# Performance work log

Hardware: AMD Instinct MI355X
Metric: run time of the kernel (lower is better)

Reference implementation:

```python
import jax, jax.numpy as jnp
import numpy as np
from jax import lax

HEATMAP_THRESH = 0.1


def _conv(x, w, b, stride=1):
    y = lax.conv_general_dilated(x, w, (stride, stride), 'SAME',
                                 dimension_numbers=('NCHW', 'OIHW', 'NCHW'))
    return y + b[None, :, None, None]


def _maxpool2(x):
    return lax.reduce_window(x, -jnp.inf, lax.max, (1, 1, 2, 2), (1, 1, 2, 2), 'VALID')


def _up2(x):
    return jnp.repeat(jnp.repeat(x, 2, axis=2), 2, axis=3)


def _find_peaks_mask(hm, thresh):
    # Vectorized equivalent of the CPU nested-loop _find_peaks:
    # interior pixel is a peak iff v > thresh and v >= its 4 axial neighbors.
    c = hm[:, :, 1:-1, 1:-1]
    m = ((c > thresh)
         & (c >= hm[:, :, :-2, 1:-1]) & (c >= hm[:, :, 2:, 1:-1])
         & (c >= hm[:, :, 1:-1, :-2]) & (c >= hm[:, :, 1:-1, 2:]))
    return jnp.pad(m, ((0, 0), (0, 0), (1, 1), (1, 1)))  # border never a peak


def _param(key, shape):
    fan_in = int(np.prod(shape[1:]))
    return jax.random.normal(key, shape, jnp.float32) / np.sqrt(fan_in)


_SHAPES = {
    'w_d1': (32, 3, 3, 3), 'w_d2': (64, 32, 3, 3), 'w_bn': (128, 64, 3, 3),
    'w_u1': (64, 192, 3, 3), 'w_u2': (32, 96, 3, 3), 'w_seg': (1, 32, 1, 1),
    'w_p1': (64, 4, 3, 3), 'w_p2': (128, 64, 3, 3),
    'w_hm': (17, 128, 1, 1), 'w_paf': (32, 128, 1, 1),
}


def setup_inputs() -> dict:
    key = jax.random.key(0)
    ks = jax.random.split(key, 1 + len(_SHAPES))
    B, H, W = 8, 384, 384
    inp = {'x': jax.random.normal(ks[0], (B, 3, H, W), jnp.float32)}
    for i, (n, s) in enumerate(_SHAPES.items()):
        inp[n] = _param(ks[i + 1], s)
        inp[n.replace('w_', 'b_')] = jnp.zeros((s[0],), jnp.float32)
    return inp


def _forward(x, w_d1, b_d1, w_d2, b_d2, w_bn, b_bn, w_u1, b_u1, w_u2, b_u2,
             w_seg, b_seg, w_p1, b_p1, w_p2, b_p2, w_hm, b_hm, w_paf, b_paf):
    # --- UNet segmentation ---
    d1 = jax.nn.relu(_conv(x, w_d1, b_d1))                    # [B,32,384,384]
    d2 = jax.nn.relu(_conv(_maxpool2(d1), w_d2, b_d2))        # [B,64,192,192]
    bn = jax.nn.relu(_conv(_maxpool2(d2), w_bn, b_bn))        # [B,128,96,96]
    u1 = jax.nn.relu(_conv(jnp.concatenate([_up2(bn), d2], 1), w_u1, b_u1))  # [B,64,192,192]
    u2 = jax.nn.relu(_conv(jnp.concatenate([_up2(u1), d1], 1), w_u2, b_u2))  # [B,32,384,384]
    seg = _conv(u2, w_seg, b_seg)                             # [B,1,384,384]
    # --- Pose net on image + detached seg logits ---
    xp = jnp.concatenate([x, lax.stop_gradient(seg)], axis=1)  # detach()
    p1 = jax.nn.relu(_conv(xp, w_p1, b_p1, stride=2))          # [B,64,192,192]
    p2 = jax.nn.relu(_conv(p1, w_p2, b_p2, stride=2))          # [B,128,96,96]
    hm = _conv(p2, w_hm, b_hm)                                 # [B,17,96,96]
    paf = _conv(p2, w_paf, b_paf)                              # [B,32,96,96]
    return seg, hm, paf


def reference(x, w_d1, b_d1, w_d2, b_d2, w_bn, b_bn, w_u1, b_u1, w_u2, b_u2,
              w_seg, b_seg, w_p1, b_p1, w_p2, b_p2, w_hm, b_hm, w_paf, b_paf):
    seg, hm, paf = _forward(x, w_d1, b_d1, w_d2, b_d2, w_bn, b_bn, w_u1, b_u1,
                            w_u2, b_u2, w_seg, b_seg, w_p1, b_p1, w_p2, b_p2,
                            w_hm, b_hm, w_paf, b_paf)
    # jit-friendly replacement for the variable-length python peak lists:
    # boolean mask over [B,K,h,w]; (x,y) coords recoverable via jnp.nonzero offline.
    peaks = _find_peaks_mask(hm, HEATMAP_THRESH)
    return seg, hm, paf, peaks
```

## Files before the change

kernel.cpp:

```cpp
#include <hip/hip_runtime.h>


#define BS 256
#define BSW 512

typedef _Float16 half8 __attribute__((ext_vector_type(8)));
typedef float floatx4 __attribute__((ext_vector_type(4)));

#define LDSDW 20
#define PLT8 10000
#define PLT4 6000
#define ESTR 388
#define ESTR4 196

__device__ inline void packw_gen_body(
    const float* __restrict__ w, _Float16* __restrict__ bp, int Cin, int Cout,
    int tid, int total)
{
    int lane = tid & 63;
    int t = tid >> 6;
    int NTl = Cout >> 4;
    int nt = t % NTl; t /= NTl;
    int tap = t % 9;
    int chunk = t / 9;
    int q = lane >> 4, n = lane & 15;
    int co = nt * 16 + n;
    _Float16* ph = bp + (size_t)tid * 8;
    _Float16* pl = bp + (size_t)total * 8 + (size_t)tid * 8;
#pragma unroll
    for (int j = 0; j < 8; ++j) {
        int ci = chunk * 32 + q * 8 + j;
        float v = w[((size_t)co * Cin + ci) * 9 + tap];
        _Float16 h = (_Float16)v;
        ph[j] = h;
        pl[j] = (_Float16)(v - (float)h);
    }
}

__device__ inline void packw_1x1_body(
    const float* __restrict__ w, _Float16* __restrict__ bp, int Cin, int NTl, int Cout,
    int tid, int total)
{
    int lane = tid & 63;
    int t = tid >> 6;
    int nt = t % NTl;
    int chunk = t / NTl;
    int q = lane >> 4, n = lane & 15;
    int co = nt * 16 + n;
    _Float16* ph = bp + (size_t)tid * 8;
    _Float16* pl = bp + (size_t)total * 8 + (size_t)tid * 8;
#pragma unroll
    for (int j = 0; j < 8; ++j) {
        int ci = chunk * 32 + q * 8 + j;
        float v = (co < Cout) ? w[(size_t)co * Cin + ci] : 0.f;
        _Float16 h = (_Float16)v;
        ph[j] = h;
        pl[j] = (_Float16)(v - (float)h);
    }
}

__global__ __launch_bounds__(BS) void packw_all_kernel(
    const float* __restrict__ w_u1, const float* __restrict__ w_u2,
    const float* __restrict__ w_d2, const float* __restrict__ w_bn,
    const float* __restrict__ w_p2, const float* __restrict__ w_hm,
    const float* __restrict__ w_paf,
    _Float16* __restrict__ bp_u1, _Float16* __restrict__ bp_u2,
    _Float16* __restrict__ bp_d2, _Float16* __restrict__ bp_bn,
    _Float16* __restrict__ bp_p2, _Float16* __restrict__ bp_hm,
    _Float16* __restrict__ bp_paf)
{
    int tid = blockIdx.x * BS + threadIdx.x;
    if (tid < 13824) { packw_gen_body(w_u1, bp_u1, 192, 64, tid, 13824); return; }
    tid -= 13824;
    if (tid < 3456)  { packw_gen_body(w_u2, bp_u2, 96, 32, tid, 3456); return; }
    tid -= 3456;
    if (tid < 2304)  { packw_gen_body(w_d2, bp_d2, 32, 64, tid, 2304); return; }
    tid -= 2304;
    if (tid < 9216)  { packw_gen_body(w_bn, bp_bn, 64, 128, tid, 9216); return; }
    tid -= 9216;
    if (tid < 9216)  { packw_gen_body(w_p2, bp_p2, 64, 128, tid, 9216); return; }
    tid -= 9216;
    if (tid < 512)   { packw_1x1_body(w_hm, bp_hm, 128, 2, 17, tid, 512); return; }
    tid -= 512;
    if (tid < 512)   { packw_1x1_body(w_paf, bp_paf, 128, 2, 32, tid, 512); return; }
}

template <int TCO>
__global__ __launch_bounds__(BS, 2) void conv3x3_pool_kernel(
    const float* __restrict__ inA, int Ca,
    const float* __restrict__ w, const float* __restrict__ b,
    _Float16* __restrict__ oph, _Float16* __restrict__ opl,
    int N, int H, int W, int Cout)
{
    const int W8 = W >> 3;
    const int H2 = H >> 1, W2 = W >> 1;
    int idx = blockIdx.x * BS + threadIdx.x;
    int total = N * H2 * W8;
    if (idx >= total) return;
    int x8 = idx % W8;
    int t  = idx / W8;
    int yo = t % H2;
    int n  = t / H2;
    int x0 = x8 << 3;
    const int co0 = blockIdx.y * TCO;
    const bool left_ok  = (x0 > 0);
    const bool right_ok = (x0 + 8 < W);
    const int Cin = Ca;

    float pool[TCO][4];

#pragma unroll
    for (int rr = 0; rr < 2; ++rr) {
        int y = 2 * yo + rr;
        float acc[TCO][8];
#pragma unroll
        for (int j = 0; j < TCO; ++j) {
            float bv = b[co0 + j];
#pragma unroll
            for (int p = 0; p < 8; ++p) acc[j][p] = bv;
        }

        for (int ci = 0; ci < Cin; ++ci) {
            float v[3][10];
#pragma unroll
            for (int ky = 0; ky < 3; ++ky) {
                int iy = y + ky - 1;
                if (iy < 0 || iy >= H) {
#pragma unroll
                    for (int p = 0; p < 10; ++p) v[ky][p] = 0.f;
                    continue;
                }
                const float* r = inA + ((size_t)(n * Ca + ci) * H + iy) * W;
                v[ky][0] = left_ok ? r[x0 - 1] : 0.f;
                float4 q0 = *(const float4*)(r + x0);
                float4 q1 = *(const float4*)(r + x0 + 4);
                v[ky][1] = q0.x; v[ky][2] = q0.y; v[ky][3] = q0.z; v[ky][4] = q0.w;
                v[ky][5] = q1.x; v[ky][6] = q1.y; v[ky][7] = q1.z; v[ky][8] = q1.w;
                v[ky][9] = right_ok ? r[x0 + 8] : 0.f;
            }
#pragma unroll
            for (int j = 0; j < TCO; ++j) {
                const float* wp = w + ((size_t)(co0 + j) * Cin + ci) * 9;
#pragma unroll
                for (int ky = 0; ky < 3; ++ky) {
                    float w0 = wp[ky * 3 + 0], w1 = wp[ky * 3 + 1], w2 = wp[ky * 3 + 2];
#pragma unroll
                    for (int p = 0; p < 8; ++p)
                        acc[j][p] += w0 * v[ky][p] + w1 * v[ky][p + 1] + w2 * v[ky][p + 2];
                }
            }
        }

#pragma unroll
        for (int j = 0; j < TCO; ++j) {
#pragma unroll
            for (int p4 = 0; p4 < 4; ++p4) {
                float mrow = fmaxf(fmaxf(acc[j][2 * p4], 0.f),
                                   fmaxf(acc[j][2 * p4 + 1], 0.f));
                pool[j][p4] = (rr == 0) ? mrow : fmaxf(pool[j][p4], mrow);
            }
        }
    }

#pragma unroll
    for (int p4 = 0; p4 < 4; ++p4) {
        half8 hv, lv;
#pragma unroll
        for (int j = 0; j < 8; ++j) {
            float v = pool[j][p4];
            _Float16 h = (_Float16)v;
            hv[j] = h;
            lv[j] = (_Float16)(v - (float)h);
        }
        size_t oa = ((size_t)((n * (Cout >> 3) + (co0 >> 3)) * H2 + yo) * W2
                     + (x0 >> 1) + p4) * 8;
        *(half8*)(oph + oa) = hv;
        *(half8*)(opl + oa) = lv;
    }
}

template <int CHUNKS, int NT, int HH, int WW, int OUTMODE>
__global__ __launch_bounds__(BS) void conv3x3s_mfma_kernel(
    const _Float16* __restrict__ inh, const _Float16* __restrict__ inl,
    const _Float16* __restrict__ bp,
    const float* __restrict__ bias,
    _Float16* __restrict__ osph,
    _Float16* __restrict__ ospl)
{
    constexpr int PL = 4 * 34 * LDSDW;
    constexpr int EPI = 64 * NT * 16;
    constexpr int LDS_DW = (2 * PL > EPI) ? 2 * PL : EPI;
    __shared__ unsigned int lds[LDS_DW];

    int xblks = WW / 32;
    int b = blockIdx.x;
    int xb = b % xblks; b /= xblks;
    int yp = b % (HH / 2);
    int n  = b / (HH / 2);
    int y0 = yp * 2;
    int x0 = xb * 32;

    int tid = threadIdx.x;
    int lane = tid & 63, wv = tid >> 6;
    int m = lane & 15, q = lane >> 4;
    int lrow = wv >> 1;
    int lx   = (wv & 1) * 16;

    floatx4 acc[NT];
#pragma unroll
    for (int nt = 0; nt < NT; ++nt) acc[nt] = (floatx4){0.f, 0.f, 0.f, 0.f};

    const int planeW = CHUNKS * 9 * NT * 64 * 8;

    for (int chunk = 0; chunk < CHUNKS; ++chunk) {
        __syncthreads();
        for (int e = tid; e < 4 * 34 * 4; e += BS) {
            int xi = e % 34;
            int rest = e / 34;
            int oct = rest & 3;
            int row = rest >> 2;
            int iy = y0 - 1 + row, gx = x0 - 1 + xi;
            half8 hv = {}, lv = {};
            if (iy >= 0 && iy < HH && gx >= 0 && gx < WW) {
                size_t ga = ((size_t)((n * (CHUNKS * 4) + chunk * 4 + oct) * HH + iy) * WW + gx) * 8;
                hv = *(const half8*)(inh + ga);
                lv = *(const half8*)(inl + ga);
            }
            int base = (row * 34 + xi) * LDSDW + oct * 4;
            *(half8*)((char*)lds + (size_t)base * 4) = hv;
            *(half8*)((char*)lds + ((size_t)PL + base) * 4) = lv;
        }
        __syncthreads();
#pragma unroll
        for (int ky = 0; ky < 3; ++ky) {
#pragma unroll
            for (int kx = 0; kx < 3; ++kx) {
                int row = lrow + ky;
                int xi  = lx + m + kx;
                int adw = (row * 34 + xi) * LDSDW + q * 4;
                half8 ah = *(const half8*)((const char*)lds + (size_t)adw * 4);
                half8 al = *(const half8*)((const char*)lds + ((size_t)PL + adw) * 4);
                int tap = ky * 3 + kx;
                const _Float16* bpp = bp + ((size_t)(chunk * 9 + tap) * NT) * 64 * 8;
#pragma unroll
                for (int nt = 0; nt < NT; ++nt) {
                    half8 bh = *(const half8*)(bpp + ((size_t)nt * 64 + lane) * 8);
                    half8 bl = *(const half8*)(bpp + planeW + ((size_t)nt * 64 + lane) * 8);
                    acc[nt] = __builtin_amdgcn_mfma_f32_16x16x32_f16(ah, bh, acc[nt], 0, 0, 0);
                    acc[nt] = __builtin_amdgcn_mfma_f32_16x16x32_f16(ah, bl, acc[nt], 0, 0, 0);
                    acc[nt] = __builtin_amdgcn_mfma_f32_16x16x32_f16(al, bh, acc[nt], 0, 0, 0);
                }
            }
        }
    }

    __syncthreads();
#pragma unroll
    for (int nt = 0; nt < NT; ++nt) {
#pragma unroll
        for (int r = 0; r < 4; ++r) {
            int co = nt * 16 + m;
            int pxl = wv * 16 + q * 4 + r;
            ((float*)lds)[co * 64 + pxl] = acc[nt][r];
        }
    }
    __syncthreads();
    {
        constexpr int OCTS = NT * 2;
        for (int it = tid; it < OCTS * 64; it += BS) {
            int px = it & 63;
            int oct = it >> 6;
            int row = y0 + (px >> 5), xx = x0 + (px & 31);
            half8 hv, lv;
#pragma unroll
            for (int j = 0; j < 8; ++j) {
                float v = fmaxf(((float*)lds)[(oct * 8 + j) * 64 + px] + bias[oct * 8 + j], 0.f);
                _Float16 hh = (_Float16)v;
                hv[j] = hh;
                lv[j] = (_Float16)(v - (float)hh);
            }
            size_t oaddr = ((size_t)((n * OCTS + oct) * HH + row) * WW + xx) * 8;
            *(half8*)(osph + oaddr) = hv;
            *(half8*)(ospl + oaddr) = lv;
        }
    }
}

__global__ __launch_bounds__(BS) void d2_mfma4_kernel(
    const _Float16* __restrict__ inh, const _Float16* __restrict__ inl,
    const _Float16* __restrict__ bp,
    const float* __restrict__ bias,
    _Float16* __restrict__ oh, _Float16* __restrict__ ol_,
    _Float16* __restrict__ oph, _Float16* __restrict__ opl)
{
    __shared__ unsigned int lds[2 * PLT4 + 128];
    const int Ho = 192, Wo = 192;
    int b = blockIdx.x;
    int xb = b % 4; b /= 4;
    int yb = b % 48;
    int n  = b / 48;
    int y0 = yb * 4;
    int x0 = xb * 48;

    int tid = threadIdx.x;
    int lane = tid & 63, wv = tid >> 6;
    int m = lane & 15, q = lane >> 4;

    floatx4 acc[3][4];
#pragma unroll
    for (int mt = 0; mt < 3; ++mt)
#pragma unroll
        for (int nt = 0; nt < 4; ++nt) acc[mt][nt] = (floatx4){0.f, 0.f, 0.f, 0.f};

    for (int e = tid; e < 6 * 50 * 4; e += BS) {
        int xi = e % 50;
        int rest = e / 50;
        int oct = rest & 3;
        int row = rest >> 2;
        int iy = y0 - 1 + row, gx = x0 - 1 + xi;
        half8 hv = {}, lv = {};
        if (iy >= 0 && iy < Ho && gx >= 0 && gx < Wo) {
            size_t ga = ((size_t)((n * 4 + oct) * Ho + iy) * Wo + gx) * 8;
            hv = *(const half8*)(inh + ga);
            lv = *(const half8*)(inl + ga);
        }
        int base = (row * 50 + xi) * LDSDW + oct * 4;
        *(half8*)((char*)lds + (size_t)base * 4) = hv;
        *(half8*)((char*)lds + ((size_t)PLT4 + base) * 4) = lv;
    }
    __syncthreads();
#pragma unroll
    for (int ky = 0; ky < 3; ++ky) {
#pragma unroll
        for (int kx = 0; kx < 3; ++kx) {
            int tap = ky * 3 + kx;
            const _Float16* bpp = bp + (size_t)tap * 2048;
            half8 bh[4], bl[4];
#pragma unroll
            for (int nt = 0; nt < 4; ++nt) {
                bh[nt] = *(const half8*)(bpp + ((size_t)nt * 64 + lane) * 8);
                bl[nt] = *(const half8*)(bpp + 18432 + ((size_t)nt * 64 + lane) * 8);
            }
            int row = wv + ky;
#pragma unroll
            for (int mt = 0; mt < 3; ++mt) {
                int px = 16 * mt + m;
                int xi = px + kx;
                int adw = (row * 50 + xi) * LDSDW + q * 4;
                half8 ah = *(const half8*)((const char*)lds + (size_t)adw * 4);
                half8 al = *(const half8*)((const char*)lds + ((size_t)PLT4 + adw) * 4);
#pragma unroll
                for (int nt = 0; nt < 4; ++nt) {
                    acc[mt][nt] = __builtin_amdgcn_mfma_f32_16x16x32_f16(ah, bh[nt], acc[mt][nt], 0, 0, 0);
                    acc[mt][nt] = __builtin_amdgcn_mfma_f32_16x16x32_f16(ah, bl[nt], acc[mt][nt], 0, 0, 0);
                    acc[mt][nt] = __builtin_amdgcn_mfma_f32_16x16x32_f16(al, bh[nt], acc[mt][nt], 0, 0, 0);
                }
            }
        }
    }

#pragma unroll
    for (int h = 0; h < 2; ++h) {
        __syncthreads();
#pragma unroll
        for (int ntl = 0; ntl < 2; ++ntl) {
#pragma unroll
            for (int mt = 0; mt < 3; ++mt) {
#pragma unroll
                for (int r = 0; r < 4; ++r) {
                    ((float*)lds)[(ntl * 16 + m) * ESTR4 + wv * 48 + 16 * mt + q * 4 + r]
                        = acc[mt][h * 2 + ntl][r];
                }
            }
        }
        __syncthreads();
        for (int it = tid; it < 4 * 192; it += BS) {
            int px = it % 192;
            int ol = it / 192;
            int row = y0 + px / 48, xx = x0 + px % 48;
            half8 hv, lv;
#pragma unroll
            for (int j = 0; j < 8; ++j) {
                int col = ol * 8 + j;
                float v = fmaxf(((float*)lds)[col * ESTR4 + px] + bias[h * 32 + col], 0.f);
                _Float16 hh = (_Float16)v;
                hv[j] = hh;
                lv[j] = (_Float16)(v - (float)hh);
            }
            size_t oaddr = ((size_t)((n * 8 + h * 4 + ol) * Ho + row) * Wo + xx) * 8;
            *(half8*)(oh + oaddr) = hv;
            *(half8*)(ol_ + oaddr) = lv;
        }
        for (int it = tid; it < 4 * 2 * 24; it += BS) {
            int xo = it % 24;
            int rest = it / 24;
            int ro = rest & 1;
            int ol = rest >> 1;
            half8 hv, lv;
#pragma unroll
            for (int j = 0; j < 8; ++j) {
                int col = ol * 8 + j;
                float bb = bias[h * 32 + col];
                const float* buf = (const float*)lds + col * ESTR4;
                float t0 = fmaxf(fmaxf(buf[(2 * ro) * 48 + 2 * xo] + bb, 0.f),
                                 fmaxf(buf[(2 * ro) * 48 + 2 * xo + 1] + bb, 0.f));
                float t1 = fmaxf(fmaxf(buf[(2 * ro + 1) * 48 + 2 * xo] + bb, 0.f),
                                 fmaxf(buf[(2 * ro + 1) * 48 + 2 * xo + 1] + bb, 0.f));
                float v = fmaxf(t0, t1);
                _Float16 hh = (_Float16)v;
                hv[j] = hh;
                lv[j] = (_Float16)(v - (float)hh);
            }
            size_t oaddr = ((size_t)((n * 8 + h * 4 + ol) * 96 + (yb * 2 + ro)) * 96
                            + (xb * 24 + xo)) * 8;
            *(half8*)(oph + oaddr) = hv;
            *(half8*)(opl + oaddr) = lv;
        }
    }
}

template <int CHUNKS, int NT, int WI>
__global__ __launch_bounds__(BS) void conv3x3s2s_mfma_kernel(
    const _Float16* __restrict__ inh, const _Float16* __restrict__ inl,
    const _Float16* __restrict__ bp,
    const float* __restrict__ bias,
    _Float16* __restrict__ oh, _Float16* __restrict__ ol_)
{
    constexpr int WO = WI / 2;
    constexpr int PLs = 5 * 68 * LDSDW;
    constexpr int EPI = 64 * NT * 16;
    constexpr int LDS_DW = (2 * PLs > EPI) ? 2 * PLs : EPI;
    __shared__ unsigned int lds[LDS_DW];

    int xblks = WO / 32;
    int b = blockIdx.x;
    int xb = b % xblks; b /= xblks;
    int yp = b % (WO / 2);
    int n  = b / (WO / 2);
    int y0 = yp * 2;
    int x0 = xb * 32;

    int tid = threadIdx.x;
    int lane = tid & 63, wv = tid >> 6;
    int m = lane & 15, q = lane >> 4;
    int lrow = wv >> 1;
    int lx   = (wv & 1) * 16;

    floatx4 acc[NT];
#pragma unroll
    for (int nt = 0; nt < NT; ++nt) acc[nt] = (floatx4){0.f, 0.f, 0.f, 0.f};

    const int planeW = CHUNKS * 9 * NT * 64 * 8;

    for (int chunk = 0; chunk < CHUNKS; ++chunk) {
        __syncthreads();
        for (int e = tid; e < 5 * 68 * 4; e += BS) {
            int xi = e % 68;
            int rest = e / 68;
            int oct = rest & 3;
            int row = rest >> 2;
            int iy = 2 * y0 + row, ix = 2 * x0 + xi;
            half8 hv = {}, lv = {};
            if (xi < 65 && iy < WI && ix < WI) {
                size_t ga = ((size_t)((n * (CHUNKS * 4) + chunk * 4 + oct) * WI + iy) * WI + ix) * 8;
                hv = *(const half8*)(inh + ga);
                lv = *(const half8*)(inl + ga);
            }
            int pos = (xi & 1) * 34 + (xi >> 1);
            int base = (row * 68 + pos) * LDSDW + oct * 4;
            *(half8*)((char*)lds + (size_t)base * 4) = hv;
            *(half8*)((char*)lds + ((size_t)PLs + base) * 4) = lv;
        }
        __syncthreads();
#pragma unroll
        for (int ky = 0; ky < 3; ++ky) {
#pragma unroll
            for (int kx = 0; kx < 3; ++kx) {
                int row = 2 * lrow + ky;
                int pos = (kx & 1) * 34 + (lx + m) + (kx >> 1);
                int adw = (row * 68 + pos) * LDSDW + q * 4;
                half8 ah = *(const half8*)((const char*)lds + (size_t)adw * 4);
                half8 al = *(const half8*)((const char*)lds + ((size_t)PLs + adw) * 4);
                int tap = ky * 3 + kx;
                const _Float16* bpp = bp + ((size_t)(chunk * 9 + tap) * NT) * 64 * 8;
#pragma unroll
                for (int nt = 0; nt < NT; ++nt) {
                    half8 bh = *(const half8*)(bpp + ((size_t)nt * 64 + lane) * 8);
                    half8 bl = *(const half8*)(bpp + planeW + ((size_t)nt * 64 + lane) * 8);
                    acc[nt] = __builtin_amdgcn_mfma_f32_16x16x32_f16(ah, bh, acc[nt], 0, 0, 0);
                    acc[nt] = __builtin_amdgcn_mfma_f32_16x16x32_f16(ah, bl, acc[nt], 0, 0, 0);
                    acc[nt] = __builtin_amdgcn_mfma_f32_16x16x32_f16(al, bh, acc[nt], 0, 0, 0);
                }
            }
        }
    }

    __syncthreads();
#pragma unroll
    for (int nt = 0; nt < NT; ++nt) {
#pragma unroll
        for (int r = 0; r < 4; ++r) {
            int co = nt * 16 + m;
            int pxl = wv * 16 + q * 4 + r;
            ((float*)lds)[co * 64 + pxl] = acc[nt][r];
        }
    }
    __syncthreads();
    {
        constexpr int OCTS = NT * 2;
        for (int it = tid; it < OCTS * 64; it += BS) {
            int px = it & 63;
            int oct = it >> 6;
            int row = y0 + (px >> 5), xx = x0 + (px & 31);
            half8 hv, lv;
#pragma unroll
            for (int j = 0; j < 8; ++j) {
                float v = fmaxf(((float*)lds)[(oct * 8 + j) * 64 + px] + bias[oct * 8 + j], 0.f);
                _Float16 hh = (_Float16)v;
                hv[j] = hh;
                lv[j] = (_Float16)(v - (float)hh);
            }
            size_t oaddr = ((size_t)((n * OCTS + oct) * WO + row) * WO + xx) * 8;
            *(half8*)(oh + oaddr) = hv;
            *(half8*)(ol_ + oaddr) = lv;
        }
    }
}

__global__ __launch_bounds__(BS) void conv1x1_heads_kernel(
    const _Float16* __restrict__ inh, const _Float16* __restrict__ inl,
    const _Float16* __restrict__ bph, const _Float16* __restrict__ bpp,
    const float* __restrict__ bh_, const float* __restrict__ bpf,
    float* __restrict__ out_hm, float* __restrict__ out_paf, int HW)
{
    constexpr int PL1 = 64 * LDSDW;
    __shared__ unsigned int lds[64 * 64];

    int pblks = HW / 64;
    int b = blockIdx.x;
    int pb = b % pblks;
    int n  = b / pblks;
    int sp0 = pb * 64;

    int tid = threadIdx.x;
    int lane = tid & 63, wv = tid >> 6;
    int m = lane & 15, q = lane >> 4;

    floatx4 acc[4];
#pragma unroll
    for (int nt = 0; nt < 4; ++nt) acc[nt] = (floatx4){0.f, 0.f, 0.f, 0.f};

    for (int chunk = 0; chunk < 4; ++chunk) {
        __syncthreads();
        {
            int px = tid & 63;
            int oct = tid >> 6;
            size_t ga = (((size_t)(n * 16 + chunk * 4 + oct)) * HW + sp0 + px) * 8;
            half8 hv = *(const half8*)(inh + ga);
            half8 lv = *(const half8*)(inl + ga);
            int base = px * LDSDW + oct * 4;
            *(half8*)((char*)lds + (size_t)base * 4) = hv;
            *(half8*)((char*)lds + ((size_t)PL1 + base) * 4) = lv;
        }
        __syncthreads();
        {
            int adw = (wv * 16 + m) * LDSDW + q * 4;
            half8 ah = *(const half8*)((const char*)lds + (size_t)adw * 4);
            half8 al = *(const half8*)((const char*)lds + ((size_t)PL1 + adw) * 4);
#pragma unroll
            for (int nt = 0; nt < 4; ++nt) {
                const _Float16* base = (nt < 2) ? bph : bpp;
                int ntl = nt & 1;
                const _Float16* pbh = base + (size_t)(chunk * 2 + ntl) * 512 + (size_t)lane * 8;
                half8 bh = *(const half8*)pbh;
                half8 bl = *(const half8*)(pbh + 4096);
                acc[nt] = __builtin_amdgcn_mfma_f32_16x16x32_f16(ah, bh, acc[nt], 0, 0, 0);
                acc[nt] = __builtin_amdgcn_mfma_f32_16x16x32_f16(ah, bl, acc[nt], 0, 0, 0);
                acc[nt] = __builtin_amdgcn_mfma_f32_16x16x32_f16(al, bh, acc[nt], 0, 0, 0);
            }
        }
    }

    __syncthreads();
#pragma unroll
    for (int nt = 0; nt < 4; ++nt) {
#pragma unroll
        for (int r = 0; r < 4; ++r) {
            ((float*)lds)[(nt * 16 + m) * 64 + wv * 16 + q * 4 + r] = acc[nt][r];
        }
    }
    __syncthreads();
    {
        int co = tid >> 2;
        int g  = tid & 3;
        const float* lp = (const float*)lds + co * 64 + g * 16;
        if (co < 17) {
            float bb = bh_[co];
            float* op = out_hm + ((size_t)(n * 17 + co)) * HW + sp0 + g * 16;
#pragma unroll
            for (int u = 0; u < 16; u += 4) {
                float4 vv = *(const float4*)(lp + u);
                vv.x += bb; vv.y += bb; vv.z += bb; vv.w += bb;
                *(float4*)(op + u) = vv;
            }
        } else if (co >= 32) {
            int pco = co - 32;
            float bb = bpf[pco];
            float* op = out_paf + ((size_t)(n * 32 + pco)) * HW + sp0 + g * 16;
#pragma unroll
            for (int u = 0; u < 16; u += 4) {
                float4 vv = *(const float4*)(lp + u);
                vv.x += bb; vv.y += bb; vv.z += bb; vv.w += bb;
                *(float4*)(op + u) = vv;
            }
        }
    }
}

__global__ __launch_bounds__(BS) void u1_mfma_kernel(
    const _Float16* __restrict__ bnh, const _Float16* __restrict__ bnl,
    const _Float16* __restrict__ d2h, const _Float16* __restrict__ d2l,
    const _Float16* __restrict__ bp,
    const float* __restrict__ b_u1,
    _Float16* __restrict__ oh, _Float16* __restrict__ ol_)
{
    __shared__ unsigned int lds[2 * PLT4 + 128];
    const int Ho = 192, Wo = 192;
    int b = blockIdx.x;
    int xb = b % 4; b /= 4;
    int yb = b % 48;
    int n  = b / 48;
    int y0 = yb * 4;
    int x0 = xb * 48;

    int tid = threadIdx.x;
    int lane = tid & 63, wv = tid >> 6;
    int m = lane & 15, q = lane >> 4;
    int yr = y0 + wv;

    floatx4 acc[3][4];
#pragma unroll
    for (int mt = 0; mt < 3; ++mt)
#pragma unroll
        for (int nt = 0; nt < 4; ++nt) acc[mt][nt] = (floatx4){0.f, 0.f, 0.f, 0.f};

    const int hh0 = (y0 - 1) >> 1;
    const int hx0 = (x0 - 1) >> 1;

    for (int chunk = 0; chunk < 6; ++chunk) {
        __syncthreads();
        if (chunk < 4) {
            for (int e = tid; e < 4 * 26 * 4; e += BS) {
                int xi = e % 26;
                int rest = e / 26;
                int oct = rest & 3;
                int row = rest >> 2;
                int hy = hh0 + row, hx = hx0 + xi;
                half8 hv = {}, lv = {};
                if (hy >= 0 && hy < 96 && hx >= 0 && hx < 96) {
                    size_t ga = ((size_t)((n * 16 + chunk * 4 + oct) * 96 + hy) * 96 + hx) * 8;
                    hv = *(const half8*)(bnh + ga);
                    lv = *(const half8*)(bnl + ga);
                }
                int base = (row * 50 + xi) * LDSDW + oct * 4;
                *(half8*)((char*)lds + (size_t)base * 4) = hv;
                *(half8*)((char*)lds + ((size_t)PLT4 + base) * 4) = lv;
            }
        } else {
            for (int e = tid; e < 6 * 50 * 4; e += BS) {
                int xi = e % 50;
                int rest = e / 50;
                int oct = rest & 3;
                int row = rest >> 2;
                int iy = y0 - 1 + row, gx = x0 - 1 + xi;
                half8 hv = {}, lv = {};
                if (iy >= 0 && iy < Ho && gx >= 0 && gx < Wo) {
                    size_t ga = ((size_t)((n * 8 + (chunk - 4) * 4 + oct) * Ho + iy) * Wo + gx) * 8;
                    hv = *(const half8*)(d2h + ga);
                    lv = *(const half8*)(d2l + ga);
                }
                int base = (row * 50 + xi) * LDSDW + oct * 4;
                *(half8*)((char*)lds + (size_t)base * 4) = hv;
                *(half8*)((char*)lds + ((size_t)PLT4 + base) * 4) = lv;
            }
        }
        __syncthreads();
#pragma unroll
        for (int ky = 0; ky < 3; ++ky) {
#pragma unroll
            for (int kx = 0; kx < 3; ++kx) {
                int tap = ky * 3 + kx;
                const _Float16* bpp = bp + ((size_t)(chunk * 9 + tap) * 4) * 64 * 8;
                half8 bh[4], bl[4];
#pragma unroll
                for (int nt = 0; nt < 4; ++nt) {
                    bh[nt] = *(const half8*)(bpp + ((size_t)nt * 64 + lane) * 8);
                    bl[nt] = *(const half8*)(bpp + 110592 + ((size_t)nt * 64 + lane) * 8);
                }
                int row;
                if (chunk < 4) row = ((yr + ky - 1) >> 1) - hh0;
                else           row = wv + ky;
#pragma unroll
                for (int mt = 0; mt < 3; ++mt) {
                    int px = 16 * mt + m;
                    int xi = (chunk < 4) ? (((x0 + px + kx - 1) >> 1) - hx0)
                                         : (px + kx);
                    int adw = (row * 50 + xi) * LDSDW + q * 4;
                    half8 ah = *(const half8*)((const char*)lds + (size_t)adw * 4);
                    half8 al = *(const half8*)((const char*)lds + ((size_t)PLT4 + adw) * 4);
#pragma unroll
                    for (int nt = 0; nt < 4; ++nt) {
                        acc[mt][nt] = __builtin_amdgcn_mfma_f32_16x16x32_f16(ah, bh[nt], acc[mt][nt], 0, 0, 0);
                        acc[mt][nt] = __builtin_amdgcn_mfma_f32_16x16x32_f16(ah, bl[nt], acc[mt][nt], 0, 0, 0);
                        acc[mt][nt] = __builtin_amdgcn_mfma_f32_16x16x32_f16(al, bh[nt], acc[mt][nt], 0, 0, 0);
                    }
                }
            }
        }
    }

#pragma unroll
    for (int h = 0; h < 2; ++h) {
        __syncthreads();
#pragma unroll
        for (int ntl = 0; ntl < 2; ++ntl) {
#pragma unroll
            for (int mt = 0; mt < 3; ++mt) {
#pragma unroll
                for (int r = 0; r < 4; ++r) {
                    ((float*)lds)[(ntl * 16 + m) * ESTR4 + wv * 48 + 16 * mt + q * 4 + r]
                        = acc[mt][h * 2 + ntl][r];
                }
            }
        }
        __syncthreads();
        for (int it = tid; it < 4 * 192; it += BS) {
            int px = it % 192;
            int ol = it / 192;
            int row = y0 + px / 48, xx = x0 + px % 48;
            half8 hv, lv;
#pragma unroll
            for (int j = 0; j < 8; ++j) {
                int col = ol * 8 + j;
                float v = fmaxf(((float*)lds)[col * ESTR4 + px] + b_u1[h * 32 + col], 0.f);
                _Float16 hh = (_Float16)v;
                hv[j] = hh;
                lv[j] = (_Float16)(v - (float)hh);
            }
            size_t oaddr = ((size_t)((n * 8 + h * 4 + ol) * Ho + row) * Wo + xx) * 8;
            *(half8*)(oh + oaddr) = hv;
            *(half8*)(ol_ + oaddr) = lv;
        }
    }
}

__global__ __launch_bounds__(BSW) void u2seg_mfma_kernel(
    const _Float16* __restrict__ u1h, const _Float16* __restrict__ u1l,
    const _Float16* __restrict__ d1h, const _Float16* __restrict__ d1l,
    const _Float16* __restrict__ bp,
    const float* __restrict__ b_u2,
    const float* __restrict__ w_seg,
    const float* __restrict__ b_seg,
    float* __restrict__ seg)
{
    __shared__ unsigned int lds[2 * PLT8];
    const int Ho = 384, Wo = 384;
    int b = blockIdx.x;
    int xb = b % 8; b /= 8;
    int yb = b % 48;
    int n  = b / 48;
    int y0 = yb * 8;
    int x0 = xb * 48;

    int tid = threadIdx.x;
    int lane = tid & 63, wv = tid >> 6;
    int m = lane & 15, q = lane >> 4;
    int yr = y0 + wv;

    floatx4 acc[3][2];
#pragma unroll
    for (int mt = 0; mt < 3; ++mt) {
        acc[mt][0] = (floatx4){0.f, 0.f, 0.f, 0.f};
        acc[mt][1] = (floatx4){0.f, 0.f, 0.f, 0.f};
    }

    const int hh0 = (y0 - 1) >> 1;
    const int hx0 = (x0 - 1) >> 1;

    for (int chunk = 0; chunk < 3; ++chunk) {
        __syncthreads();
        if (chunk < 2) {
            for (int e = tid; e < 6 * 26 * 4; e += BSW) {
                int xi = e % 26;
                int rest = e / 26;
                int oct = rest & 3;
                int row = rest >> 2;
                int hy = hh0 + row, hx = hx0 + xi;
                half8 hv = {}, lv = {};
                if (hy >= 0 && hy < 192 && hx >= 0 && hx < 192) {
                    size_t ga = ((size_t)((n * 8 + chunk * 4 + oct) * 192 + hy) * 192 + hx) * 8;
                    hv = *(const half8*)(u1h + ga);
                    lv = *(const half8*)(u1l + ga);
                }
                int base = (row * 50 + xi) * LDSDW + oct * 4;
                *(half8*)((char*)lds + (size_t)base * 4) = hv;
                *(half8*)((char*)lds + ((size_t)PLT8 + base) * 4) = lv;
            }
        } else {
            for (int e = tid; e < 10 * 50 * 4; e += BSW) {
                int xi = e % 50;
                int rest = e / 50;
                int oct = rest & 3;
                int row = rest >> 2;
                int iy = y0 - 1 + row, gx = x0 - 1 + xi;
                half8 hv = {}, lv = {};
                if (iy >= 0 && iy < Ho && gx >= 0 && gx < Wo) {
                    size_t ga = ((size_t)((n * 4 + oct) * Ho + iy) * Wo + gx) * 8;
                    hv = *(const half8*)(d1h + ga);
                    lv = *(const half8*)(d1l + ga);
                }
                int base = (row * 50 + xi) * LDSDW + oct * 4;
                *(half8*)((char*)lds + (size_t)base * 4) = hv;
                *(half8*)((char*)lds + ((size_t)PLT8 + base) * 4) = lv;
            }
        }
        __syncthreads();
#pragma unroll
        for (int ky = 0; ky < 3; ++ky) {
#pragma unroll
            for (int kx = 0; kx < 3; ++kx) {
                int tap = ky * 3 + kx;
                const _Float16* bpp = bp + ((size_t)(chunk * 9 + tap) * 2) * 64 * 8;
                half8 bh0 = *(const half8*)(bpp + (size_t)lane * 8);
                half8 bl0 = *(const half8*)(bpp + 27648 + (size_t)lane * 8);
                half8 bh1 = *(const half8*)(bpp + ((size_t)64 + lane) * 8);
                half8 bl1 = *(const half8*)(bpp + 27648 + ((size_t)64 + lane) * 8);
                int row;
                if (chunk < 2) row = ((yr + ky - 1) >> 1) - hh0;
                else           row = wv + ky;
#pragma unroll
                for (int mt = 0; mt < 3; ++mt) {
                    int px = 16 * mt + m;
                    int xi = (chunk < 2) ? (((x0 + px + kx - 1) >> 1) - hx0)
                                         : (px + kx);
                    int adw = (row * 50 + xi) * LDSDW + q * 4;
                    half8 ah = *(const half8*)((const char*)lds + (size_t)adw * 4);
                    half8 al = *(const half8*)((const char*)lds + ((size_t)PLT8 + adw) * 4);
                    acc[mt][0] = __builtin_amdgcn_mfma_f32_16x16x32_f16(ah, bh0, acc[mt][0], 0, 0, 0);
                    acc[mt][0] = __builtin_amdgcn_mfma_f32_16x16x32_f16(ah, bl0, acc[mt][0], 0, 0, 0);
                    acc[mt][0] = __builtin_amdgcn_mfma_f32_16x16x32_f16(al, bh0, acc[mt][0], 0, 0, 0);
                    acc[mt][1] = __builtin_amdgcn_mfma_f32_16x16x32_f16(ah, bh1, acc[mt][1], 0, 0, 0);
                    acc[mt][1] = __builtin_amdgcn_mfma_f32_16x16x32_f16(ah, bl1, acc[mt][1], 0, 0, 0);
                    acc[mt][1] = __builtin_amdgcn_mfma_f32_16x16x32_f16(al, bh1, acc[mt][1], 0, 0, 0);
                }
            }
        }
    }

    float bb0 = b_u2[m], bb1 = b_u2[16 + m];
    float ws0 = w_seg[m], ws1 = w_seg[16 + m];
    float bseg = b_seg[0];
#pragma unroll
    for (int mt = 0; mt < 3; ++mt) {
        float sr[4];
#pragma unroll
        for (int r = 0; r < 4; ++r) {
            float p = ws0 * fmaxf(acc[mt][0][r] + bb0, 0.f)
                    + ws1 * fmaxf(acc[mt][1][r] + bb1, 0.f);
            p += __shfl_xor(p, 1);
            p += __shfl_xor(p, 2);
            p += __shfl_xor(p, 4);
            p += __shfl_xor(p, 8);
            sr[r] = p + bseg;
        }
        if (m == 0) {
            float4 o; o.x = sr[0]; o.y = sr[1]; o.z = sr[2]; o.w = sr[3];
            *(float4*)(seg + ((size_t)n * Ho + yr) * Wo + x0 + 16 * mt + q * 4) = o;
        }
    }
}


template <int UPA, int TCO, int SPLIT>
__global__ __launch_bounds__(BS, 2) void conv3x3_x8_kernel(
    const float* __restrict__ inA, int Ca,
    const float* __restrict__ inB, int Cb,
    const float* __restrict__ w, const float* __restrict__ b,
    float* __restrict__ out,
    int N, int H, int W, int Cout, int do_relu,
    _Float16* __restrict__ osph, _Float16* __restrict__ ospl)
{
    const int W8 = W >> 3;
    int idx = blockIdx.x * BS + threadIdx.x;
    int total = N * H * W8;
    if (idx >= total) return;
    int x8 = idx % W8;
    int t  = idx / W8;
    int y  = t % H;
    int n  = t / H;
    int x0 = x8 << 3;
    const int co0 = blockIdx.y * TCO;
    const bool left_ok  = (x0 > 0);
    const bool right_ok = (x0 + 8 < W);
    const int Cin = Ca + Cb;

    float acc[TCO][8];
#pragma unroll
    for (int j = 0; j < TCO; ++j) {
        float bv = b[co0 + j];
#pragma unroll
        for (int p = 0; p < 8; ++p) acc[j][p] = bv;
    }

    for (int ci = 0; ci < Cin; ++ci) {
        float v[3][10];
#pragma unroll
        for (int ky = 0; ky < 3; ++ky) {
            int iy = y + ky - 1;
            if (iy < 0 || iy >= H) {
#pragma unroll
                for (int p = 0; p < 10; ++p) v[ky][p] = 0.f;
                continue;
            }
            if (UPA == 2 && ci < Ca) {
                const float* r = inA + ((size_t)(n * Ca + ci) * (H >> 1) + (iy >> 1)) * (W >> 1);
                int xh = x0 >> 1;
                float sm = left_ok  ? r[xh - 1] : 0.f;
                float4 qq = *(const float4*)(r + xh);
                float s4 = right_ok ? r[xh + 4] : 0.f;
                v[ky][0] = sm;
                v[ky][1] = qq.x; v[ky][2] = qq.x;
                v[ky][3] = qq.y; v[ky][4] = qq.y;
                v[ky][5] = qq.z; v[ky][6] = qq.z;
                v[ky][7] = qq.w; v[ky][8] = qq.w;
                v[ky][9] = s4;
            } else {
                const float* r = (ci < Ca)
                    ? inA + ((size_t)(n * Ca + ci) * H + iy) * W
                    : inB + ((size_t)(n * Cb + (ci - Ca)) * H + iy) * W;
                v[ky][0] = left_ok ? r[x0 - 1] : 0.f;
                float4 q0 = *(const float4*)(r + x0);
                float4 q1 = *(const float4*)(r + x0 + 4);
                v[ky][1] = q0.x; v[ky][2] = q0.y; v[ky][3] = q0.z; v[ky][4] = q0.w;
                v[ky][5] = q1.x; v[ky][6] = q1.y; v[ky][7] = q1.z; v[ky][8] = q1.w;
                v[ky][9] = right_ok ? r[x0 + 8] : 0.f;
            }
        }
#pragma unroll
        for (int j = 0; j < TCO; ++j) {
            const float* wp = w + ((size_t)(co0 + j) * Cin + ci) * 9;
#pragma unroll
            for (int ky = 0; ky < 3; ++ky) {
                float w0 = wp[ky * 3 + 0], w1 = wp[ky * 3 + 1], w2 = wp[ky * 3 + 2];
#pragma unroll
                for (int p = 0; p < 8; ++p)
                    acc[j][p] += w0 * v[ky][p] + w1 * v[ky][p + 1] + w2 * v[ky][p + 2];
            }
        }
    }

    if (SPLIT) {
#pragma unroll
        for (int p = 0; p < 8; ++p) {
            half8 hv, lv;
#pragma unroll
            for (int j = 0; j < 8; ++j) {
                float v = acc[j][p];
                if (do_relu) v = fmaxf(v, 0.f);
                _Float16 hh = (_Float16)v;
                hv[j] = hh;
                lv[j] = (_Float16)(v - (float)hh);
            }
            size_t oaddr = ((size_t)((n * (Cout >> 3) + (co0 >> 3)) * H + y) * W + x0 + p) * 8;
            *(half8*)(osph + oaddr) = hv;
            *(half8*)(ospl + oaddr) = lv;
        }
    } else {
#pragma unroll
        for (int j = 0; j < TCO; ++j) {
#pragma unroll
            for (int p = 0; p < 8; ++p)
                if (do_relu) acc[j][p] = fmaxf(acc[j][p], 0.f);
            float* o = out + ((size_t)(n * Cout + co0 + j) * H + y) * W + x0;
            float4 q0; q0.x = acc[j][0]; q0.y = acc[j][1]; q0.z = acc[j][2]; q0.w = acc[j][3];
            float4 q1; q1.x = acc[j][4]; q1.y = acc[j][5]; q1.z = acc[j][6]; q1.w = acc[j][7];
            *(float4*)o = q0;
            *(float4*)(o + 4) = q1;
        }
    }
}

template <int TCO, int SPLIT>
__global__ __launch_bounds__(BS) void conv3x3_s2_co_kernel(
    const float* __restrict__ inA, int Ca,
    const float* __restrict__ inB, int Cb,
    const float* __restrict__ w, const float* __restrict__ b,
    float* __restrict__ out,
    int N, int Hi, int Wi, int Cout, int do_relu,
    _Float16* __restrict__ osph, _Float16* __restrict__ ospl)
{
    const int Ho = Hi >> 1, Wo = Wi >> 1, Woq = Wo >> 2;
    int idx = blockIdx.x * BS + threadIdx.x;
    int total = N * Ho * Woq;
    if (idx >= total) return;
    int q  = idx % Woq;
    int t  = idx / Woq;
    int oy = t % Ho;
    int n  = t / Ho;
    int ox0 = q << 2;
    int ix0 = ox0 << 1;
    const int co0 = blockIdx.y * TCO;
    const bool right_ok = (ix0 + 8 < Wi);
    const int Cin = Ca + Cb;

    float acc[TCO][4];
#pragma unroll
    for (int j = 0; j < TCO; ++j) {
        float bv = b[co0 + j];
        acc[j][0] = bv; acc[j][1] = bv; acc[j][2] = bv; acc[j][3] = bv;
    }

    for (int ci = 0; ci < Cin; ++ci) {
        const float* base = (ci < Ca)
            ? inA + (size_t)(n * Ca + ci) * Hi * Wi
            : inB + (size_t)(n * Cb + (ci - Ca)) * Hi * Wi;
        float v[3][9];
#pragma unroll
        for (int ky = 0; ky < 3; ++ky) {
            int iy = 2 * oy + ky;
            if (iy >= Hi) {
#pragma unroll
                for (int p = 0; p < 9; ++p) v[ky][p] = 0.f;
                continue;
            }
            const float* r = base + (size_t)iy * Wi + ix0;
            float4 a = *(const float4*)r;
            float4 c = *(const float4*)(r + 4);
            v[ky][0] = a.x; v[ky][1] = a.y; v[ky][2] = a.z; v[ky][3] = a.w;
            v[ky][4] = c.x; v[ky][5] = c.y; v[ky][6] = c.z; v[ky][7] = c.w;
            v[ky][8] = right_ok ? r[8] : 0.f;
        }
#pragma unroll
        for (int j = 0; j < TCO; ++j) {
            const float* wp = w + ((size_t)(co0 + j) * Cin + ci) * 9;
#pragma unroll
            for (int ky = 0; ky < 3; ++ky) {
                float w0 = wp[ky * 3 + 0], w1 = wp[ky * 3 + 1], w2 = wp[ky * 3 + 2];
#pragma unroll
                for (int p = 0; p < 4; ++p)
                    acc[j][p] += w0 * v[ky][2 * p] + w1 * v[ky][2 * p + 1] + w2 * v[ky][2 * p + 2];
            }
        }
    }

    if (SPLIT) {
#pragma unroll
        for (int p = 0; p < 4; ++p) {
            half8 hv, lv;
#pragma unroll
            for (int j = 0; j < 8; ++j) {
                float v = acc[j][p];
                if (do_relu) v = fmaxf(v, 0.f);
                _Float16 hh = (_Float16)v;
                hv[j] = hh;
                lv[j] = (_Float16)(v - (float)hh);
            }
            size_t oaddr = ((size_t)((n * (Cout >> 3) + (co0 >> 3)) * Ho + oy) * Wo + ox0 + p) * 8;
            *(half8*)(osph + oaddr) = hv;
            *(half8*)(ospl + oaddr) = lv;
        }
    } else {
#pragma unroll
        for (int j = 0; j < TCO; ++j) {
            float4 o;
            o.x = acc[j][0]; o.y = acc[j][1]; o.z = acc[j][2]; o.w = acc[j][3];
            if (do_relu) {
                o.x = fmaxf(o.x, 0.f); o.y = fmaxf(o.y, 0.f);
                o.z = fmaxf(o.z, 0.f); o.w = fmaxf(o.w, 0.f);
            }
            *(float4*)(out + ((size_t)(n * Cout + co0 + j) * Ho + oy) * Wo + ox0) = o;
        }
    }
}

__global__ __launch_bounds__(BS) void peaks_kernel(
    const float* __restrict__ hm, float* __restrict__ out,
    int NC, int H, int W, float thresh)
{
    int idx = blockIdx.x * BS + threadIdx.x;
    int total = NC * H * W;
    if (idx >= total) return;
    int x = idx % W;
    int t = idx / W;
    int y = t % H;
    int c = t / H;
    float r = 0.f;
    if (x >= 1 && x < W - 1 && y >= 1 && y < H - 1) {
        const float* base = hm + (size_t)c * H * W;
        float cv = base[y * W + x];
        if (cv > thresh &&
            cv >= base[(y - 1) * W + x] &&
            cv >= base[(y + 1) * W + x] &&
            cv >= base[y * W + (x - 1)] &&
            cv >= base[y * W + (x + 1)])
            r = 1.f;
    }
    out[idx] = r;
}

static inline int nblk(long n) { return (int)((n + BS - 1) / BS); }

extern "C" void kernel_launch(void* const* d_in, const int* in_sizes, int n_in,
                              void* d_out, int out_size, void* d_ws, size_t ws_size,
                              hipStream_t stream)
{
    const float* x     = (const float*)d_in[0];
    const float* w_d1  = (const float*)d_in[1];  const float* b_d1  = (const float*)d_in[2];
    const float* w_d2  = (const float*)d_in[3];  const float* b_d2  = (const float*)d_in[4];
    const float* w_bn  = (const float*)d_in[5];  const float* b_bn  = (const float*)d_in[6];
    const float* w_u1  = (const float*)d_in[7];  const float* b_u1  = (const float*)d_in[8];
    const float* w_u2  = (const float*)d_in[9];  const float* b_u2  = (const float*)d_in[10];
    const float* w_seg = (const float*)d_in[11]; const float* b_seg = (const float*)d_in[12];
    const float* w_p1  = (const float*)d_in[13]; const float* b_p1  = (const float*)d_in[14];
    const float* w_p2  = (const float*)d_in[15]; const float* b_p2  = (const float*)d_in[16];
    const float* w_hm  = (const float*)d_in[17]; const float* b_hm  = (const float*)d_in[18];
    const float* w_paf = (const float*)d_in[19]; const float* b_paf = (const float*)d_in[20];

    const int N = 8, H = 384, W = 384;
    const int H2 = 192, W2 = 192, H4 = 96, W4 = 96;

    float* ws = (float*)d_ws;
    _Float16* pd1sp_h = (_Float16*)(ws);
    _Float16* pd1sp_l = (_Float16*)(ws + 4718592);
    _Float16* d2sp_h = (_Float16*)(ws + 28311552);
    _Float16* d2sp_l = (_Float16*)(ws + 37748736);
    _Float16* pd2sp_h = (_Float16*)(ws + 47185920);
    _Float16* pd2sp_l = (_Float16*)(ws + 49545216);
    _Float16* bnsp_h = (_Float16*)(ws + 18874368);
    _Float16* bnsp_l = (_Float16*)(ws + 23592960);
    _Float16* u1sp_h = (_Float16*)(ws);
    _Float16* u1sp_l = (_Float16*)(ws + 9437184);
    _Float16* d1sp_h = (_Float16*)(ws + 18874368);
    _Float16* d1sp_l = (_Float16*)(ws + 37748736);
    _Float16* p1sp_h = (_Float16*)(ws);
    _Float16* p1sp_l = (_Float16*)(ws + 9437184);
    _Float16* p2sp_h = (_Float16*)(ws + 18874368);
    _Float16* p2sp_l = (_Float16*)(ws + 23592960);

    float* out_seg   = (float*)d_out;
    float* out_hm    = out_seg + 1179648;
    float* out_paf   = out_hm + 1253376;
    float* out_peaks = out_paf + 2359296;
    _Float16* bp_u1  = (_Float16*)(out_seg + 4792320);
    _Float16* bp_u2  = (_Float16*)(out_seg + 4902912);
    _Float16* bp_d2  = (_Float16*)(out_seg + 4930560);
    _Float16* bp_bn  = (_Float16*)(out_seg + 4948992);
    _Float16* bp_p2  = (_Float16*)(out_seg + 5022720);
    _Float16* bp_hm  = (_Float16*)(out_seg + 5096448);
    _Float16* bp_paf = (_Float16*)(out_seg + 5100544);

    packw_all_kernel<<<nblk(39040), BS, 0, stream>>>(
        w_u1, w_u2, w_d2, w_bn, w_p2, w_hm, w_paf,
        bp_u1, bp_u2, bp_d2, bp_bn, bp_p2, bp_hm, bp_paf);
    {
        dim3 g(nblk((long)N * H2 * (W / 8)), 32 / 8);
        conv3x3_pool_kernel<8><<<g, BS, 0, stream>>>(
            x, 3, w_d1, b_d1, pd1sp_h, pd1sp_l, N, H, W, 32);
    }
    d2_mfma4_kernel<<<8 * 48 * 4, BS, 0, stream>>>(
        pd1sp_h, pd1sp_l, bp_d2, b_d2, d2sp_h, d2sp_l, pd2sp_h, pd2sp_l);
    conv3x3s_mfma_kernel<2, 8, 96, 96, 1><<<8 * 48 * 3, BS, 0, stream>>>(
        pd2sp_h, pd2sp_l, bp_bn, b_bn, bnsp_h, bnsp_l);
    u1_mfma_kernel<<<8 * 48 * 4, BS, 0, stream>>>(
        bnsp_h, bnsp_l, d2sp_h, d2sp_l, bp_u1, b_u1, u1sp_h, u1sp_l);
    {
        dim3 g(nblk((long)N * H * (W / 8)), 32 / 8);
        conv3x3_x8_kernel<1, 8, 1><<<g, BS, 0, stream>>>(
            x, 3, nullptr, 0, w_d1, b_d1, nullptr, N, H, W, 32, 1, d1sp_h, d1sp_l);
    }
    u2seg_mfma_kernel<<<8 * 48 * 8, BSW, 0, stream>>>(
        u1sp_h, u1sp_l, d1sp_h, d1sp_l, bp_u2, b_u2, w_seg, b_seg, out_seg);
    {
        dim3 g(nblk((long)N * H2 * (W2 / 4)), 64 / 8);
        conv3x3_s2_co_kernel<8, 1><<<g, BS, 0, stream>>>(
            x, 3, out_seg, 1, w_p1, b_p1, nullptr, N, H, W, 64, 1, p1sp_h, p1sp_l);
    }
    conv3x3s2s_mfma_kernel<2, 8, 192><<<8 * 48 * 3, BS, 0, stream>>>(
        p1sp_h, p1sp_l, bp_p2, b_p2, p2sp_h, p2sp_l);
    conv1x1_heads_kernel<<<8 * 144, BS, 0, stream>>>(
        p2sp_h, p2sp_l, bp_hm, bp_paf, b_hm, b_paf, out_hm, out_paf, H4 * W4);
    peaks_kernel<<<nblk((long)N * 17 * H4 * W4), BS, 0, stream>>>(
        out_hm, out_peaks, N * 17, H4, W4, 0.1f);
}
```

Baseline: 854.9 us.

## Fuse weight packing into pooled d1 conv launch and widen p1 channel tile

The separate weight-packing kernel is merged with the first pooled 3x3 conv into one launch. Extra blocks appended after the conv grid do the packing, with the conv's problem dims hardcoded. This removes one kernel launch and lets packing overlap the conv. Separately, the stride-2 p1 conv now computes 16 output channels per thread instead of 8, halving the grid's y-dimension and the re-reading of input rows, at the cost of more registers per thread.

```diff
diff --git a/kernel.cpp b/kernel.cpp
--- a/kernel.cpp
+++ b/kernel.cpp
@@ -59,7 +59,10 @@
     }
 }
 
-__global__ __launch_bounds__(BS) void packw_all_kernel(
+__global__ __launch_bounds__(BS, 2) void pool_packw_kernel(
+    const float* __restrict__ inA,
+    const float* __restrict__ w, const float* __restrict__ b,
+    _Float16* __restrict__ oph, _Float16* __restrict__ opl,
     const float* __restrict__ w_u1, const float* __restrict__ w_u2,
     const float* __restrict__ w_d2, const float* __restrict__ w_bn,
     const float* __restrict__ w_p2, const float* __restrict__ w_hm,
@@ -69,32 +72,34 @@
     _Float16* __restrict__ bp_p2, _Float16* __restrict__ bp_hm,
     _Float16* __restrict__ bp_paf)
 {
-    int tid = blockIdx.x * BS + threadIdx.x;
-    if (tid < 13824) { packw_gen_body(w_u1, bp_u1, 192, 64, tid, 13824); return; }
-    tid -= 13824;
-    if (tid < 3456)  { packw_gen_body(w_u2, bp_u2, 96, 32, tid, 3456); return; }
-    tid -= 3456;
-    if (tid < 2304)  { packw_gen_body(w_d2, bp_d2, 32, 64, tid, 2304); return; }
-    tid -= 2304;
-    if (tid < 9216)  { packw_gen_body(w_bn, bp_bn, 64, 128, tid, 9216); return; }
-    tid -= 9216;
-    if (tid < 9216)  { packw_gen_body(w_p2, bp_p2, 64, 128, tid, 9216); return; }
-    tid -= 9216;
-    if (tid < 512)   { packw_1x1_body(w_hm, bp_hm, 128, 2, 17, tid, 512); return; }
-    tid -= 512;
-    if (tid < 512)   { packw_1x1_body(w_paf, bp_paf, 128, 2, 32, tid, 512); return; }
-}
-
-template <int TCO>
-__global__ __launch_bounds__(BS, 2) void conv3x3_pool_kernel(
-    const float* __restrict__ inA, int Ca,
-    const float* __restrict__ w, const float* __restrict__ b,
-    _Float16* __restrict__ oph, _Float16* __restrict__ opl,
-    int N, int H, int W, int Cout)
-{
+    const int N = 8, H = 384, W = 384, Cout = 32, Ca = 3;
+    const int POOLX = 288;
+    const int POOLBLKS = POOLX * 4;
+    int blk = blockIdx.x;
+    if (blk >= POOLBLKS) {
+        int tid = (blk - POOLBLKS) * BS + threadIdx.x;
+        if (tid < 13824) { packw_gen_body(w_u1, bp_u1, 192, 64, tid, 13824); return; }
+        tid -= 13824;
+        if (tid < 3456)  { packw_gen_body(w_u2, bp_u2, 96, 32, tid, 3456); return; }
+        tid -= 3456;
+        if (tid < 2304)  { packw_gen_body(w_d2, bp_d2, 32, 64, tid, 2304); return; }
+        tid -= 2304;
+        if (tid < 9216)  { packw_gen_body(w_bn, bp_bn, 64, 128, tid, 9216); return; }
+        tid -= 9216;
+        if (tid < 9216)  { packw_gen_body(w_p2, bp_p2, 64, 128, tid, 9216); return; }
+        tid -= 9216;
+        if (tid < 512)   { packw_1x1_body(w_hm, bp_hm, 128, 2, 17, tid, 512); return; }
+        tid -= 512;
+        if (tid < 512)   { packw_1x1_body(w_paf, bp_paf, 128, 2, 32, tid, 512); return; }
+        return;
+    }
+
+    const int TCO = 8;
     const int W8 = W >> 3;
     const int H2 = H >> 1, W2 = W >> 1;
-    int idx = blockIdx.x * BS + threadIdx.x;
+    int bx = blk % POOLX;
+    int by = blk / POOLX;
+    int idx = bx * BS + threadIdx.x;
     int total = N * H2 * W8;
     if (idx >= total) return;
     int x8 = idx % W8;
@@ -102,7 +107,7 @@
     int yo = t % H2;
     int n  = t / H2;
     int x0 = x8 << 3;
-    const int co0 = blockIdx.y * TCO;
+    const int co0 = by * TCO;
     const bool left_ok  = (x0 > 0);
     const bool right_ok = (x0 + 8 < W);
     const int Cin = Ca;
@@ -961,19 +966,22 @@
 
     if (SPLIT) {
 #pragma unroll
-        for (int p = 0; p < 8; ++p) {
-            half8 hv, lv;
-#pragma unroll
-            for (int j = 0; j < 8; ++j) {
-                float v = acc[j][p];
-                if (do_relu) v = fmaxf(v, 0.f);
-                _Float16 hh = (_Float16)v;
-                hv[j] = hh;
-                lv[j] = (_Float16)(v - (float)hh);
-            }
-            size_t oaddr = ((size_t)((n * (Cout >> 3) + (co0 >> 3)) * H + y) * W + x0 + p) * 8;
-            *(half8*)(osph + oaddr) = hv;
-            *(half8*)(ospl + oaddr) = lv;
+        for (int oo = 0; oo < TCO / 8; ++oo) {
+#pragma unroll
+            for (int p = 0; p < 8; ++p) {
+                half8 hv, lv;
+#pragma unroll
+                for (int j = 0; j < 8; ++j) {
+                    float v = acc[oo * 8 + j][p];
+                    if (do_relu) v = fmaxf(v, 0.f);
+                    _Float16 hh = (_Float16)v;
+                    hv[j] = hh;
+                    lv[j] = (_Float16)(v - (float)hh);
+                }
+                size_t oaddr = ((size_t)((n * (Cout >> 3) + (co0 >> 3) + oo) * H + y) * W + x0 + p) * 8;
+                *(half8*)(osph + oaddr) = hv;
+                *(half8*)(ospl + oaddr) = lv;
+            }
         }
     } else {
 #pragma unroll
@@ -1055,19 +1063,22 @@
 
     if (SPLIT) {
 #pragma unroll
-        for (int p = 0; p < 4; ++p) {
-            half8 hv, lv;
-#pragma unroll
-            for (int j = 0; j < 8; ++j) {
-                float v = acc[j][p];
-                if (do_relu) v = fmaxf(v, 0.f);
-                _Float16 hh = (_Float16)v;
-                hv[j] = hh;
-                lv[j] = (_Float16)(v - (float)hh);
-            }
-            size_t oaddr = ((size_t)((n * (Cout >> 3) + (co0 >> 3)) * Ho + oy) * Wo + ox0 + p) * 8;
-            *(half8*)(osph + oaddr) = hv;
-            *(half8*)(ospl + oaddr) = lv;
+        for (int oo = 0; oo < TCO / 8; ++oo) {
+#pragma unroll
+            for (int p = 0; p < 4; ++p) {
+                half8 hv, lv;
+#pragma unroll
+                for (int j = 0; j < 8; ++j) {
+                    float v = acc[oo * 8 + j][p];
+                    if (do_relu) v = fmaxf(v, 0.f);
+                    _Float16 hh = (_Float16)v;
+                    hv[j] = hh;
+                    lv[j] = (_Float16)(v - (float)hh);
+                }
+                size_t oaddr = ((size_t)((n * (Cout >> 3) + (co0 >> 3) + oo) * Ho + oy) * Wo + ox0 + p) * 8;
+                *(half8*)(osph + oaddr) = hv;
+                *(half8*)(ospl + oaddr) = lv;
+            }
         }
     } else {
 #pragma unroll
@@ -1159,14 +1170,10 @@
     _Float16* bp_hm  = (_Float16*)(out_seg + 5096448);
     _Float16* bp_paf = (_Float16*)(out_seg + 5100544);
 
-    packw_all_kernel<<<nblk(39040), BS, 0, stream>>>(
+    pool_packw_kernel<<<1152 + 153, BS, 0, stream>>>(
+        x, w_d1, b_d1, pd1sp_h, pd1sp_l,
         w_u1, w_u2, w_d2, w_bn, w_p2, w_hm, w_paf,
         bp_u1, bp_u2, bp_d2, bp_bn, bp_p2, bp_hm, bp_paf);
-    {
-        dim3 g(nblk((long)N * H2 * (W / 8)), 32 / 8);
-        conv3x3_pool_kernel<8><<<g, BS, 0, stream>>>(
-            x, 3, w_d1, b_d1, pd1sp_h, pd1sp_l, N, H, W, 32);
-    }
     d2_mfma4_kernel<<<8 * 48 * 4, BS, 0, stream>>>(
         pd1sp_h, pd1sp_l, bp_d2, b_d2, d2sp_h, d2sp_l, pd2sp_h, pd2sp_l);
     conv3x3s_mfma_kernel<2, 8, 96, 96, 1><<<8 * 48 * 3, BS, 0, stream>>>(
@@ -1181,8 +1188,8 @@
     u2seg_mfma_kernel<<<8 * 48 * 8, BSW, 0, stream>>>(
         u1sp_h, u1sp_l, d1sp_h, d1sp_l, bp_u2, b_u2, w_seg, b_seg, out_seg);
     {
-        dim3 g(nblk((long)N * H2 * (W2 / 4)), 64 / 8);
-        conv3x3_s2_co_kernel<8, 1><<<g, BS, 0, stream>>>(
+        dim3 g(nblk((long)N * H2 * (W2 / 4)), 64 / 16);
+        conv3x3_s2_co_kernel<16, 1><<<g, BS, 0, stream>>>(
             x, 3, out_seg, 1, w_p1, b_p1, nullptr, N, H, W, 64, 1, p1sp_h, p1sp_l);
     }
     conv3x3s2s_mfma_kernel<2, 8, 192><<<8 * 48 * 3, BS, 0, stream>>>(
```

Measured after the change: 831.8 us. 1.03x faster.
